# Performance work log

Measured on AMD Instinct MI355X. Metric: run time of the kernel, lower is better.

## Reference

```python
import jax, jax.numpy as jnp
import numpy as np

B = 32          # patients
D = 128         # hidden dim (modality_embedding_dim == total_hidden_dim)
H = 4           # attention heads
DH = D // H     # per-head dim
L = 2           # num_graph_layers
N = {'ct': 1024, 'pet': 1024, 'clin': 256, 'gen': 2048, 'pat': 1}
# (src_type, dst_type) for the 8 relation types registered in _setup_relations
REL = [('ct','ct'), ('pet','pet'), ('clin','clin'), ('gen','gen'),
       ('pat','clin'), ('ct','gen'), ('pet','gen'), ('gen','pat')]
E_REL = [8192, 8192, 2048, 16384, 256, 8192, 8192, 2048]
EDGE_NAMES = ['e_ct','e_pet','e_clin','e_gen','e_pat2clin','e_ct2gen','e_pet2gen','e_gen2pat']


def setup_inputs() -> dict:
    key = jax.random.key(0)
    ks = iter(jax.random.split(key, 64))
    nk = lambda: next(ks)
    inp = {}
    inp['x_ct']   = jax.random.normal(nk(), (B, N['ct'],  D), jnp.float32)
    inp['x_pet']  = jax.random.normal(nk(), (B, N['pet'], D), jnp.float32)
    inp['x_clin'] = jax.random.normal(nk(), (B, N['clin'],D), jnp.float32)
    inp['x_gen']  = jax.random.normal(nk(), (B, N['gen'], D), jnp.float32)
    inp['early']  = jax.random.normal(nk(), (B, D), jnp.float32)

    def mk_edges(k, E, ns, nd):
        k1, k2 = jax.random.split(k)
        src = jax.random.randint(k1, (B, 1, E), 0, ns, jnp.int32)
        dst = jax.random.randint(k2, (B, 1, E), 0, nd, jnp.int32)
        return jnp.concatenate([src, dst], axis=1)  # [B,2,E]

    for nm, (s, d), E in zip(EDGE_NAMES, REL, E_REL):
        inp[nm] = mk_edges(nk(), E, N[s], N[d])

    sw = 1.0 / np.sqrt(D)
    inp['W_src'] = jax.random.normal(nk(), (L, 8, D, D), jnp.float32) * sw
    inp['W_dst'] = jax.random.normal(nk(), (L, 8, D, D), jnp.float32) * sw
    inp['a_src'] = jax.random.normal(nk(), (L, 8, H, DH), jnp.float32) * sw
    inp['a_dst'] = jax.random.normal(nk(), (L, 8, H, DH), jnp.float32) * sw
    inp['Wp'] = jax.random.normal(nk(), (3, D, D), jnp.float32) * sw  # CT, PET, genomic pooling
    inp['bp'] = jnp.zeros((3, D), jnp.float32)
    inp['W_sem'] = jax.random.normal(nk(), (4 * D, 128), jnp.float32) * (1.0 / np.sqrt(4 * D))
    inp['b_sem'] = jnp.zeros((128,), jnp.float32)
    inp['q_sem'] = jax.random.normal(nk(), (128,), jnp.float32) * sw
    return inp


def _leaky_relu(x):
    return jnp.where(x > 0, x, 0.2 * x)


def _gat_layer(x, edges, Ws, Wd, As, Ad):
    """One heterogeneous multi-head GAT layer summing over relation types."""
    agg = {t: jnp.zeros((B, N[t], H, DH), jnp.float32) for t in N}
    for r, ((s, d), ei) in enumerate(zip(REL, edges)):
        hs = jnp.einsum('bnd,de->bne', x[s], Ws[r]).reshape(B, N[s], H, DH)
        hd = jnp.einsum('bnd,de->bne', x[d], Wd[r]).reshape(B, N[d], H, DH)
        al_s = jnp.sum(hs * As[r], axis=-1)  # [B,Ns,H]
        al_d = jnp.sum(hd * Ad[r], axis=-1)  # [B,Nd,H]
        nd = N[d]

        def one(hs_b, as_b, ad_b, e_b):
            src, dst = e_b[0], e_b[1]
            logit = _leaky_relu(as_b[src] + ad_b[dst])                      # [E,H]
            m = jnp.full((nd, H), -1e30, logit.dtype).at[dst].max(logit)    # segment max
            p = jnp.exp(logit - m[dst])
            den = jnp.zeros((nd, H), p.dtype).at[dst].add(p)
            w = p / (den[dst] + 1e-16)                                      # edge softmax per dst node
            msg = w[:, :, None] * hs_b[src]                                 # [E,H,DH]
            return jnp.zeros((nd, H, DH), msg.dtype).at[dst].add(msg)

        agg[d] = agg[d] + jax.vmap(one)(hs, al_s, al_d, ei)
    return {t: jax.nn.elu(agg[t].reshape(B, N[t], D)) for t in N}


def _pool(feat, W, b):
    # query = Linear(mean(features)); scores = feat @ q; softmax-weighted sum
    q = jnp.mean(feat, axis=1) @ W + b            # [B,D]
    sc = jnp.einsum('bnd,bd->bn', feat, q)        # [B,N]
    w = jax.nn.softmax(sc, axis=1)
    return jnp.einsum('bn,bnd->bd', w, feat)      # [B,D]


def _forward(x_ct, x_pet, x_clin, x_gen, early, edges,
             W_src, W_dst, a_src, a_dst, Wp, bp, W_sem, b_sem, q_sem):
    x = {'ct': x_ct, 'pet': x_pet, 'clin': x_clin, 'gen': x_gen,
         'pat': early[:, None, :]}
    for l in range(L):
        x = _gat_layer(x, edges, W_src[l], W_dst[l], a_src[l], a_dst[l])
    ct_p  = _pool(x['ct'],  Wp[0], bp[0])
    pet_p = _pool(x['pet'], Wp[1], bp[1])
    gen_p = _pool(x['gen'], Wp[2], bp[2])   # shared across the 3 meta-paths
    pad = jnp.zeros((B, 2 * D), ct_p.dtype)  # pad 2D -> 4D as in original
    imm = jnp.concatenate([ct_p, gen_p, pad], axis=1)
    pro = jnp.concatenate([pet_p, gen_p, pad], axis=1)
    trt = jnp.concatenate([(ct_p + pet_p) * 0.5, gen_p, pad], axis=1)
    z = jnp.stack([imm, pro, trt], axis=1)                     # [B,3,4D]
    s = jnp.einsum('bpa,a->bp', jnp.tanh(jnp.einsum('bpf,fa->bpa', z, W_sem) + b_sem), q_sem)
    beta = jax.nn.softmax(s, axis=1)                           # [B,3]
    fused = jnp.einsum('bp,bpf->bf', beta, z)                  # [B,4D]
    return fused, beta


def reference(x_ct, x_pet, x_clin, x_gen, early,
              e_ct, e_pet, e_clin, e_gen, e_pat2clin, e_ct2gen, e_pet2gen, e_gen2pat,
              W_src, W_dst, a_src, a_dst, Wp, bp, W_sem, b_sem, q_sem):
    edges = [e_ct, e_pet, e_clin, e_gen, e_pat2clin, e_ct2gen, e_pet2gen, e_gen2pat]
    return _forward(x_ct, x_pet, x_clin, x_gen, early, edges,
                    W_src, W_dst, a_src, a_dst, Wp, bp, W_sem, b_sem, q_sem)
```

## Files before the change

kernel.cpp:

```cpp
#include <hip/hip_runtime.h>
#include <math.h>

static constexpr int NB = 32;
static constexpr int ND = 128;

typedef short bf16x8 __attribute__((ext_vector_type(8)));
typedef float f32x4  __attribute__((ext_vector_type(4)));
typedef unsigned short u16x8 __attribute__((ext_vector_type(8)));

__device__ __forceinline__ float lrelu(float x){ return x > 0.f ? x : 0.2f*x; }
__device__ __forceinline__ unsigned short f2b(float f){
  unsigned u = __float_as_uint(f);
  return (unsigned short)((u + 0x7FFFu + ((u>>16)&1u)) >> 16);
}
__device__ __forceinline__ float b2f(unsigned short b){
  return __uint_as_float(((unsigned)b) << 16);
}

__global__ __launch_bounds__(128) void k_fold(const float* __restrict__ Wsrc,
    const float* __restrict__ Wdst, const float* __restrict__ asrc,
    const float* __restrict__ adst, float* __restrict__ vbuf){
  const int wid[5] = {0,1,3,5,6};
  int lr = blockIdx.x, role = blockIdx.y, l = blockIdx.z;
  int r = wid[lr];
  const float* W = (role ? Wdst : Wsrc) + (size_t)(l*8+r)*16384;
  const float* a = (role ? adst : asrc) + (size_t)(l*8+r)*128;
  int k = threadIdx.x;
  float* o = vbuf + ((size_t)((l*5+lr)*2+role))*512 + k*4;
  #pragma unroll
  for(int h=0;h<4;h++){
    float s = 0.f;
    #pragma unroll
    for(int j=0;j<32;j++) s += W[k*128 + h*32 + j]*a[h*32 + j];
    o[h] = s;
  }
}

__global__ __launch_bounds__(256) void k_wpack(const float* __restrict__ Wsrc,
    unsigned short* __restrict__ Wf){
  const int wid[5] = {0,1,3,5,6};
  int lr = blockIdx.x, l = blockIdx.y;
  const float* W = Wsrc + (size_t)(l*8+wid[lr])*16384;
  unsigned short* o = Wf + (size_t)((l*5+lr)*4)*4096;
  for(int idx=threadIdx.x; idx<128*128; idx+=256){
    int k = idx >> 7, col = idx & 127;
    int h = col >> 5, cc = col & 31;
    int k4 = k>>2, g = k4&3, kk = k4>>3, j = 4*((k4>>2)&1) + (k&3);
    int nb = cc>>4, lane = (cc&15) + 16*g;
    o[(size_t)h*4096 + ((size_t)((kk*2+nb)*64 + lane))*8 + j] = f2b(W[k*128 + col]);
  }
}

struct CsrP {
  const int* eg[5];
  int l2E[5];
  int Nd_[5];
  int roff_[5];
  int eoff_[5];
};

__global__ __launch_bounds__(512) void k_csr(CsrP P, int* __restrict__ rowstart,
                                             int* __restrict__ srcidx){
  int b = blockIdx.x, r = blockIdx.y, t = threadIdx.x;
  int E = 1<<P.l2E[r], Nd = P.Nd_[r];
  const int* eg = P.eg[r] + (size_t)b*2*E;
  int* rsO = rowstart + P.roff_[r] + b*(Nd+1);
  int* siO = srcidx + P.eoff_[r] + (size_t)b*E;
  __shared__ int cnt[2048];
  __shared__ int stmp[512];
  for(int i=t;i<Nd;i+=512) cnt[i]=0;
  __syncthreads();
  for(int e=t;e<E;e+=512) atomicAdd(&cnt[eg[E+e]], 1);
  __syncthreads();
  int carry=0;
  for(int c0=0;c0<Nd;c0+=512){
    int idx=c0+t;
    int v=(idx<Nd)?cnt[idx]:0;
    stmp[t]=v; __syncthreads();
    for(int off=1;off<512;off<<=1){
      int u=(t>=off)?stmp[t-off]:0;
      __syncthreads();
      stmp[t]+=u;
      __syncthreads();
    }
    int excl=stmp[t]-v+carry;
    if(idx<Nd){ rsO[idx]=excl; cnt[idx]=excl; }
    int tot = stmp[511];
    __syncthreads();
    carry+=tot;
  }
  if(t==0) rsO[Nd]=carry;
  __syncthreads();
  for(int e=t;e<E;e+=512){
    int src=eg[e], dst=eg[E+e];
    int pos=atomicAdd(&cnt[dst],1);
    siO[pos]=src;
  }
}

struct HsP {
  int tb[4];
  int usef;
  const float* xf[3];
  unsigned long long xoff[3];
  int Ns[3];
  int nW[3];
  unsigned long long wfo[3][2];
  unsigned long long hso[3][2];
  unsigned long long aso[3][2];
  unsigned long long asrco[3][2];
  int nvd[3];
  unsigned long long vdo[3][3];
  unsigned long long aldo2[3][3];
  int ndd[3][3];
};

__global__ __launch_bounds__(256) void k_hs(HsP P, const unsigned short* __restrict__ x16,
    const unsigned short* __restrict__ Wf, const float* __restrict__ asrc,
    const float* __restrict__ vbuf, unsigned short* __restrict__ hs,
    float* __restrict__ als, float* __restrict__ ald){
  __shared__ unsigned short xl[16*132];
  int B = blockIdx.x;
  int t=0; while(t<2 && B>=P.tb[t+1]) t++;
  int local = B - P.tb[t];
  int b = local & 31, tile = local >> 5;
  int n0 = tile*16;
  int tid = threadIdx.x, w = tid>>6, ln = tid&63;
  if(P.usef){
    const float* xf = P.xf[t] + ((size_t)((size_t)b*P.Ns[t] + n0))*128;
    int row = tid>>4, c8 = tid&15;
    float4 a = *(const float4*)(xf + (size_t)row*128 + c8*8);
    float4 c = *(const float4*)(xf + (size_t)row*128 + c8*8 + 4);
    u16x8 r;
    r[0]=f2b(a.x); r[1]=f2b(a.y); r[2]=f2b(a.z); r[3]=f2b(a.w);
    r[4]=f2b(c.x); r[5]=f2b(c.y); r[6]=f2b(c.z); r[7]=f2b(c.w);
    *(u16x8*)&xl[row*132 + c8*8] = r;
  } else {
    int row = tid>>4, ch = tid&15;
    u16x8 v = *(const u16x8*)(x16 + P.xoff[t] + ((size_t)((size_t)b*P.Ns[t] + n0+row)*128 + ch*8));
    *(u16x8*)&xl[row*132 + ch*8] = v;
  }
  __syncthreads();
  int g = ln>>4, r15 = ln&15;
  for(int rep=0; rep<P.nW[t]; rep++){
    const unsigned short* wf = Wf + P.wfo[t][rep] + (size_t)w*4096;
    f32x4 acc[2]; acc[0]=(f32x4){0,0,0,0}; acc[1]=(f32x4){0,0,0,0};
    #pragma unroll
    for(int kk=0;kk<4;kk++){
      const unsigned short* pa = &xl[r15*132 + kk*32 + 4*g];
      ushort4 lo = *(const ushort4*)pa;
      ushort4 hi = *(const ushort4*)(pa+16);
      union { ushort u[8]; bf16x8 v; } tmp;
      tmp.u[0]=lo.x; tmp.u[1]=lo.y; tmp.u[2]=lo.z; tmp.u[3]=lo.w;
      tmp.u[4]=hi.x; tmp.u[5]=hi.y; tmp.u[6]=hi.z; tmp.u[7]=hi.w;
      bf16x8 af = tmp.v;
      #pragma unroll
      for(int nb=0;nb<2;nb++){
        bf16x8 bw = *(const bf16x8*)(wf + ((size_t)((kk*2+nb)*64 + ln))*8);
        acc[nb] = __builtin_amdgcn_mfma_f32_16x16x32_bf16(af, bw, acc[nb], 0, 0, 0);
      }
    }
    unsigned short* ho = hs + P.hso[t][rep] + ((size_t)b*P.Ns[t] + n0)*128;
    #pragma unroll
    for(int qq=0;qq<4;qq++){
      int m = 4*g + qq;
      #pragma unroll
      for(int nb=0;nb<2;nb++){
        ho[(size_t)m*128 + w*32 + nb*16 + r15] = f2b(acc[nb][qq]);
      }
    }
    {
      const float* aS = asrc + P.asrco[t][rep];
      float a0v = aS[w*32 + r15], a1v = aS[w*32 + 16 + r15];
      float p0 = acc[0][0]*a0v + acc[1][0]*a1v;
      float p1 = acc[0][1]*a0v + acc[1][1]*a1v;
      float p2 = acc[0][2]*a0v + acc[1][2]*a1v;
      float p3 = acc[0][3]*a0v + acc[1][3]*a1v;
      #pragma unroll
      for(int off=1; off<16; off<<=1){
        p0 += __shfl_xor(p0,off); p1 += __shfl_xor(p1,off);
        p2 += __shfl_xor(p2,off); p3 += __shfl_xor(p3,off);
      }
      if(r15 < 4){
        float pv = (r15==0)?p0:((r15==1)?p1:((r15==2)?p2:p3));
        als[P.aso[t][rep] + ((size_t)b*P.Ns[t] + n0 + 4*g + r15)*4 + w] = pv;
      }
    }
  }
  int nvd = P.nvd[t];
  if(tid < (nvd<<6)){
    int vd = tid>>6, rem = tid&63, row = rem>>2, h = rem&3;
    const float* vv = vbuf + P.vdo[t][vd];
    float s = 0.f;
    #pragma unroll 8
    for(int k=0;k<128;k++) s += b2f(xl[row*132+k]) * vv[k*4+h];
    ald[P.aldo2[t][vd] + ((size_t)b*P.ndd[t][vd] + n0 + row)*4 + h] = s;
  }
}

static constexpr int MAXE4 = 1536;
static constexpr int WST4  = 1548;

struct Fu5P {
  int nrel[3], ndshift[3];
  int roff[3][3], eoff[3][3], E[3][3], Ns[3][3];
  int rowbase[3][3];
  unsigned long long aldo[3][3];
  unsigned long long outoff[3];
};

__global__ __launch_bounds__(512, 8) void k_fuse5(Fu5P P,
    const int* __restrict__ rowstart, const int* __restrict__ srcidx,
    const float* __restrict__ als, const float* __restrict__ ald,
    const unsigned short* __restrict__ hs, unsigned short* __restrict__ out16){
  __shared__ float wlds[4*WST4];
  __shared__ int   silds[MAXE4];
  __shared__ float aldl[3*256];
  __shared__ int   rsl[3*65];
  __shared__ int   crs[65];
  __shared__ int   cst[3*64];
  int B = blockIdx.x;
  int xcd = B & 7, slot = B >> 3;
  int bg = slot >> 6, rem = slot & 63;
  int b = bg*8 + xcd;
  int t, dtile;
  if(rem < 32){ t = 0; dtile = rem; }
  else if(rem < 48){ t = 1; dtile = rem - 32; }
  else { t = 2; dtile = rem - 48; }
  int Nd = 1 << P.ndshift[t];
  int d0 = dtile * 64;
  int tid = threadIdx.x, w = tid>>6, ln = tid&63;
  int nrel = P.nrel[t];

  for(int q=0;q<nrel;q++){
    const int* rsq = rowstart + P.roff[t][q] + b*(Nd+1) + d0;
    for(int i=tid;i<65;i+=512) rsl[q*65+i] = rsq[i];
    const float* aldq = ald + P.aldo[t][q] + ((size_t)b*Nd + d0)*4;
    for(int i=tid;i<256;i+=512) aldl[(q<<8)+i] = aldq[i];
  }
  __syncthreads();
  if(tid < 65){
    int s = 0;
    for(int q=0;q<nrel;q++) s += rsl[q*65+tid] - rsl[q*65];
    crs[tid] = s;
  } else if(tid >= 128 && tid < 128 + nrel*64){
    int q = (tid-128)>>6, d = (tid-128)&63;
    int s = 0;
    for(int q2=0;q2<nrel;q2++) s += rsl[q2*65+d] - rsl[q2*65];
    for(int q2=0;q2<q;q2++)    s += rsl[q2*65+d+1] - rsl[q2*65+d];
    cst[q*64+d] = s;
  }
  __syncthreads();
  for(int s=tid; s<(nrel<<8); s+=512){
    int q = s>>8, r2 = s&255, dloc = r2>>2, j = r2&3;
    const int* si = srcidx + P.eoff[t][q] + (size_t)b*P.E[t][q];
    int rs0 = rsl[q*65+dloc];
    int deg = rsl[q*65+dloc+1] - rs0;
    int cb = cst[q*64+dloc];
    int bake = P.rowbase[t][q] + b*P.Ns[t][q];
    for(int i=j;i<deg;i+=4) silds[cb+i] = bake + si[rs0+i];
  }
  __syncthreads();
  for(int s=tid; s<(nrel<<8); s+=512){
    int q = s>>8, r2 = s&255, dloc = r2>>2, j = r2&3;
    int deg = rsl[q*65+dloc+1] - rsl[q*65+dloc];
    int cb = cst[q*64+dloc];
    float4 ad4 = *(const float4*)&aldl[(q<<8)+(dloc<<2)];
    for(int i=j;i<deg;i+=4){
      int e = cb+i;
      int sil = silds[e];
      float4 as4 = *(const float4*)(als + 4*(size_t)sil);
      wlds[0*WST4+e] = lrelu(as4.x+ad4.x);
      wlds[1*WST4+e] = lrelu(as4.y+ad4.y);
      wlds[2*WST4+e] = lrelu(as4.z+ad4.z);
      wlds[3*WST4+e] = lrelu(as4.w+ad4.w);
    }
  }
  __syncthreads();
  for(int s=tid; s<(nrel<<8); s+=512){
    int q = s>>8, r2 = s&255, dloc = r2>>2, h2 = r2&3;
    int e0 = cst[q*64+dloc];
    int e1 = e0 + rsl[q*65+dloc+1] - rsl[q*65+dloc];
    float* wrow = &wlds[h2*WST4];
    float m = -1e30f;
    for(int e=e0;e<e1;e++) m = fmaxf(m, wrow[e]);
    float den = 0.f;
    for(int e=e0;e<e1;e++){ float p=__expf(wrow[e]-m); wrow[e]=p; den+=p; }
    float inv = 1.f/(den + 1e-16f);
    for(int e=e0;e<e1;e++) wrow[e] *= inv;
  }
  __syncthreads();
  int h = ln>>4;
  float accA[8], accB[8];
  #pragma unroll
  for(int i=0;i<8;i++){ accA[i]=0.f; accB[i]=0.f; }
  #pragma unroll
  for(int it=0; it<8; it++){
    int dloc = w*8 + it;
    int e0 = crs[dloc], e1 = crs[dloc+1];
    float a0 = 0.f, a1 = 0.f;
    int e = e0;
    int eal = (e0+3)&~3; if(eal > e1) eal = e1;
    for(; e<eal; e++){
      float wv = wlds[h*WST4 + e];
      unsigned v = *(const unsigned*)(hs + ((size_t)silds[e]*128 + 2*ln));
      a0 += wv*__uint_as_float(v<<16);
      a1 += wv*__uint_as_float(v&0xFFFF0000u);
    }
    for(; e+8<=e1; e+=8){
      int4  sq0 = *(const int4*)&silds[e];
      int4  sq1 = *(const int4*)&silds[e+4];
      float4 wq0 = *(const float4*)&wlds[h*WST4 + e];
      float4 wq1 = *(const float4*)&wlds[h*WST4 + e + 4];
      unsigned v0 = *(const unsigned*)(hs + ((size_t)sq0.x*128 + 2*ln));
      unsigned v1 = *(const unsigned*)(hs + ((size_t)sq0.y*128 + 2*ln));
      unsigned v2 = *(const unsigned*)(hs + ((size_t)sq0.z*128 + 2*ln));
      unsigned v3 = *(const unsigned*)(hs + ((size_t)sq0.w*128 + 2*ln));
      unsigned v4 = *(const unsigned*)(hs + ((size_t)sq1.x*128 + 2*ln));
      unsigned v5 = *(const unsigned*)(hs + ((size_t)sq1.y*128 + 2*ln));
      unsigned v6 = *(const unsigned*)(hs + ((size_t)sq1.z*128 + 2*ln));
      unsigned v7 = *(const unsigned*)(hs + ((size_t)sq1.w*128 + 2*ln));
      a0 += wq0.x*__uint_as_float(v0<<16); a1 += wq0.x*__uint_as_float(v0&0xFFFF0000u);
      a0 += wq0.y*__uint_as_float(v1<<16); a1 += wq0.y*__uint_as_float(v1&0xFFFF0000u);
      a0 += wq0.z*__uint_as_float(v2<<16); a1 += wq0.z*__uint_as_float(v2&0xFFFF0000u);
      a0 += wq0.w*__uint_as_float(v3<<16); a1 += wq0.w*__uint_as_float(v3&0xFFFF0000u);
      a0 += wq1.x*__uint_as_float(v4<<16); a1 += wq1.x*__uint_as_float(v4&0xFFFF0000u);
      a0 += wq1.y*__uint_as_float(v5<<16); a1 += wq1.y*__uint_as_float(v5&0xFFFF0000u);
      a0 += wq1.z*__uint_as_float(v6<<16); a1 += wq1.z*__uint_as_float(v6&0xFFFF0000u);
      a0 += wq1.w*__uint_as_float(v7<<16); a1 += wq1.w*__uint_as_float(v7&0xFFFF0000u);
    }
    for(; e+4<=e1; e+=4){
      int4  sq = *(const int4*)&silds[e];
      float4 wq = *(const float4*)&wlds[h*WST4 + e];
      unsigned v0 = *(const unsigned*)(hs + ((size_t)sq.x*128 + 2*ln));
      unsigned v1 = *(const unsigned*)(hs + ((size_t)sq.y*128 + 2*ln));
      unsigned v2 = *(const unsigned*)(hs + ((size_t)sq.z*128 + 2*ln));
      unsigned v3 = *(const unsigned*)(hs + ((size_t)sq.w*128 + 2*ln));
      a0 += wq.x*__uint_as_float(v0<<16); a1 += wq.x*__uint_as_float(v0&0xFFFF0000u);
      a0 += wq.y*__uint_as_float(v1<<16); a1 += wq.y*__uint_as_float(v1&0xFFFF0000u);
      a0 += wq.z*__uint_as_float(v2<<16); a1 += wq.z*__uint_as_float(v2&0xFFFF0000u);
      a0 += wq.w*__uint_as_float(v3<<16); a1 += wq.w*__uint_as_float(v3&0xFFFF0000u);
    }
    for(; e<e1; e++){
      float wv = wlds[h*WST4 + e];
      unsigned v = *(const unsigned*)(hs + ((size_t)silds[e]*128 + 2*ln));
      a0 += wv*__uint_as_float(v<<16);
      a1 += wv*__uint_as_float(v&0xFFFF0000u);
    }
    accA[it] = a0; accB[it] = a1;
  }
  #pragma unroll
  for(int it=0; it<8; it++){
    int m = d0 + w*8 + it;
    float v0 = accA[it], v1 = accB[it];
    v0 = v0 > 0.f ? v0 : expm1f(v0);
    v1 = v1 > 0.f ? v1 : expm1f(v1);
    ushort2 o; o.x = f2b(v0); o.y = f2b(v1);
    *(ushort2*)(out16 + P.outoff[t] + ((size_t)b*Nd + m)*128 + 2*ln) = o;
  }
}

__device__ __constant__ const size_t POFF[3] = {0ull, 4194304ull, 8388608ull};
__device__ __constant__ const int    PNN[3]  = {1024, 1024, 2048};
static constexpr int PCH = 64;
static constexpr int MAXCH = 32;

__global__ __launch_bounds__(128) void k_pool_psum(const unsigned short* __restrict__ x2,
    float* __restrict__ part){
  int p = blockIdx.z, b = blockIdx.x, c = blockIdx.y, t = threadIdx.x;
  int Nn = PNN[p];
  if(c*PCH >= Nn) return;
  const unsigned short* f = x2 + POFF[p] + ((size_t)b*Nn + c*PCH)*ND;
  float acc = 0.f;
  #pragma unroll 8
  for(int n=0;n<PCH;n++) acc += b2f(f[(size_t)n*ND + t]);
  part[(((size_t)p*NB + b)*MAXCH + c)*ND + t] = acc;
}

__global__ __launch_bounds__(128) void k_pool_q(const float* __restrict__ part,
    const float* __restrict__ Wp, const float* __restrict__ bp,
    float* __restrict__ q){
  int p = blockIdx.z, b = blockIdx.x, t = threadIdx.x;
  int nch = PNN[p]/PCH;
  __shared__ float mean[ND];
  float s = 0.f;
  for(int c=0;c<nch;c++) s += part[(((size_t)p*NB + b)*MAXCH + c)*ND + t];
  mean[t] = s / (float)PNN[p];
  __syncthreads();
  const float* W = Wp + (size_t)p*ND*ND;
  float qv = bp[p*ND + t];
  #pragma unroll 8
  for(int k=0;k<ND;k++) qv += mean[k]*W[k*ND + t];
  q[((size_t)p*NB + b)*ND + t] = qv;
}

__global__ __launch_bounds__(256) void k_pool_score(const unsigned short* __restrict__ x2,
    const float* __restrict__ q, float* __restrict__ sc){
  int p = blockIdx.z, b = blockIdx.y;
  int w = threadIdx.x >> 6, lane = threadIdx.x & 63;
  int n = blockIdx.x*4 + w;
  int Nn = PNN[p];
  if(n >= Nn) return;
  const unsigned short* f  = x2 + POFF[p] + ((size_t)b*Nn + n)*ND;
  const float* qb = q + ((size_t)p*NB + b)*ND;
  float s = b2f(f[lane])*qb[lane] + b2f(f[lane+64])*qb[lane+64];
  #pragma unroll
  for(int off=32; off; off>>=1) s += __shfl_xor(s, off);
  if(lane == 0) sc[((size_t)p*NB + b)*2048 + n] = s;
}

__global__ __launch_bounds__(256) void k_pool_smax(const float* __restrict__ sc,
    float* __restrict__ stat){
  int p = blockIdx.z, b = blockIdx.x, t = threadIdx.x;
  int Nn = PNN[p];
  __shared__ float red[256];
  const float* s = sc + ((size_t)p*NB + b)*2048;
  float mx = -1e30f;
  for(int n=t;n<Nn;n+=256) mx = fmaxf(mx, s[n]);
  red[t] = mx; __syncthreads();
  for(int o=128;o;o>>=1){ if(t<o) red[t]=fmaxf(red[t],red[t+o]); __syncthreads(); }
  mx = red[0]; __syncthreads();
  float sum = 0.f;
  for(int n=t;n<Nn;n+=256) sum += __expf(s[n]-mx);
  red[t] = sum; __syncthreads();
  for(int o=128;o;o>>=1){ if(t<o) red[t]+=red[t+o]; __syncthreads(); }
  if(t==0){ stat[((size_t)p*NB + b)*2] = mx; stat[((size_t)p*NB + b)*2+1] = 1.f/red[0]; }
}

__global__ __launch_bounds__(128) void k_pool_wsum(const unsigned short* __restrict__ x2,
    const float* __restrict__ sc, const float* __restrict__ stat,
    float* __restrict__ part){
  int p = blockIdx.z, b = blockIdx.x, c = blockIdx.y, t = threadIdx.x;
  int Nn = PNN[p];
  if(c*PCH >= Nn) return;
  __shared__ float wsh[PCH];
  float mx  = stat[((size_t)p*NB + b)*2];
  float inv = stat[((size_t)p*NB + b)*2+1];
  if(t < PCH) wsh[t] = __expf(sc[((size_t)p*NB + b)*2048 + c*PCH + t] - mx)*inv;
  __syncthreads();
  const unsigned short* f = x2 + POFF[p] + ((size_t)b*Nn + c*PCH)*ND;
  float acc = 0.f;
  #pragma unroll 8
  for(int n=0;n<PCH;n++) acc += wsh[n]*b2f(f[(size_t)n*ND + t]);
  part[(((size_t)p*NB + b)*MAXCH + c)*ND + t] = acc;
}

__global__ __launch_bounds__(128) void k_pool_comb(const float* __restrict__ part,
    float* __restrict__ pooled){
  int p = blockIdx.z, b = blockIdx.x, t = threadIdx.x;
  int nch = PNN[p]/PCH;
  float s = 0.f;
  for(int c=0;c<nch;c++) s += part[(((size_t)p*NB + b)*MAXCH + c)*ND + t];
  pooled[((size_t)p*NB + b)*ND + t] = s;
}

__global__ __launch_bounds__(128) void k_sem(const float* __restrict__ ctp,
    const float* __restrict__ petp, const float* __restrict__ genp,
    const float* __restrict__ Wsem, const float* __restrict__ bsem,
    const float* __restrict__ qsem, float* __restrict__ fused, float* __restrict__ beta){
  int b = blockIdx.x, t = threadIdx.x;
  __shared__ float z[3][256];
  __shared__ float red[128];
  float ct = ctp[b*ND + t], pet = petp[b*ND + t], gen = genp[b*ND + t];
  z[0][t]=ct;  z[1][t]=pet; z[2][t]=0.5f*(ct+pet);
  z[0][ND+t]=gen; z[1][ND+t]=gen; z[2][ND+t]=gen;
  __syncthreads();
  float s[3];
  for(int p=0;p<3;p++){
    float a = bsem[t];
    for(int f=0;f<256;f++) a += z[p][f]*Wsem[f*128 + t];
    a = tanhf(a);
    red[t] = a * qsem[t];
    __syncthreads();
    for(int o=64;o>0;o>>=1){ if(t<o) red[t]+=red[t+o]; __syncthreads(); }
    s[p] = red[0]; __syncthreads();
  }
  float mx = fmaxf(s[0], fmaxf(s[1], s[2]));
  float e0 = __expf(s[0]-mx), e1 = __expf(s[1]-mx), e2 = __expf(s[2]-mx);
  float sm = e0+e1+e2;
  float b0 = e0/sm, b1 = e1/sm, b2 = e2/sm;
  if(t < 3) beta[b*3 + t] = (t==0)?b0:((t==1)?b1:b2);
  float f0 = b0*z[0][t] + b1*z[1][t] + b2*z[2][t];
  float f1 = b0*z[0][ND+t] + b1*z[1][ND+t] + b2*z[2][ND+t];
  fused[(size_t)b*512 + t]       = f0;
  fused[(size_t)b*512 + 128 + t] = f1;
  fused[(size_t)b*512 + 256 + t] = 0.f;
  fused[(size_t)b*512 + 384 + t] = 0.f;
}

extern "C" void kernel_launch(void* const* d_in, const int* in_sizes, int n_in,
                              void* d_out, int out_size, void* d_ws, size_t ws_size,
                              hipStream_t stream) {
  static const int wid[5]    = {0,1,3,5,6};
  static const int edgein[5] = {5,6,8,10,11};
  static const int l2E[5]    = {13,13,14,13,13};
  static const int Nd_l[5]   = {1024,1024,2048,2048,2048};
  static const int E_l[5]    = {8192,8192,16384,8192,8192};
  static const int Ns_l[5]   = {1024,1024,2048,1024,1024};
  static const int eoff[6]   = {0,262144,524288,1048576,1310720,1572864};
  static const int roff[5]   = {0,32800,65600,131168,196736};
  static const unsigned long long aoff[5]   = {0,131072,262144,524288,655360};
  static const unsigned long long aldoff[5] = {0,131072,262144,524288,786432};
  static const unsigned long long hsoff_lr[5] = {0ull,4194304ull,8388608ull,16777216ull,20971520ull};
  static const unsigned long long ALD = 786432;

  const float* Wsrc = (const float*)d_in[13];
  const float* Wp   = (const float*)d_in[17];
  const float* bp   = (const float*)d_in[18];
  const float* Wsem = (const float*)d_in[19];
  const float* bsem = (const float*)d_in[20];
  const float* qsem = (const float*)d_in[21];

  unsigned short* xc16 = (unsigned short*)d_ws;
  unsigned short* x2b16 = xc16;
  unsigned short* xmid16 = xc16 + 16777216;
  float* albase = (float*)(xmid16 + 16777216);
  float* als = albase;
  float* ald = albase + ALD;
  float* vbuf = albase + 1835008;
  unsigned short* wfbuf = (unsigned short*)(vbuf + 10240);
  float* pooled = (float*)(wfbuf + 163840);
  float* part = pooled + 12288;
  float* qbuf = part + 393216;
  float* scbuf = qbuf + 12288;
  float* stat = scbuf + 196608;
  int* rowstart = (int*)(stat + 192);
  int* srcidx = rowstart + 262304;
  unsigned short* hs16 = (unsigned short*)(srcidx + 1572864);

  { dim3 g(5,2,2); k_fold<<<g,128,0,stream>>>(Wsrc, (const float*)d_in[14],
                                              (const float*)d_in[15], (const float*)d_in[16], vbuf); }
  { dim3 g(5,2); k_wpack<<<g,256,0,stream>>>(Wsrc, wfbuf); }

  CsrP csr;
  for(int r=0;r<5;r++){
    csr.eg[r] = (const int*)d_in[edgein[r]];
    csr.l2E[r] = l2E[r]; csr.Nd_[r] = Nd_l[r];
    csr.roff_[r] = roff[r]; csr.eoff_[r] = eoff[r];
  }
  { dim3 g(NB,5); k_csr<<<g,512,0,stream>>>(csr, rowstart, srcidx); }

  static const unsigned long long xoo[3] = {0,4194304,8388608};
  static const int t2_nrel[3] = {3,1,1};
  static const int t2_lrel[3][3] = {{2,3,4},{0,0,0},{1,0,0}};
  static const int t2_nds[3] = {11,10,10};
  static const int t2_out[3] = {2,0,1};

  Fu5P fp;
  for(int t=0;t<3;t++){
    fp.nrel[t]=t2_nrel[t]; fp.ndshift[t]=t2_nds[t]; fp.outoff[t]=xoo[t2_out[t]];
    for(int q=0;q<3;q++){
      int lr = t2_lrel[t][q];
      fp.roff[t][q]=roff[lr]; fp.eoff[t][q]=eoff[lr];
      fp.E[t][q]=E_l[lr]; fp.Ns[t][q]=Ns_l[lr];
      fp.rowbase[t][q]=(int)(aoff[lr]/4);
      fp.aldo[t][q]=aldoff[lr];
    }
  }

  static const int hs_lr[3][2] = {{0,3},{1,4},{2,2}};
  static const int vd_lr[3][3] = {{0,0,0},{1,0,0},{2,3,4}};
  HsP hp;
  hp.tb[0]=0; hp.tb[1]=2048; hp.tb[2]=4096; hp.tb[3]=8192;
  hp.xf[0]=(const float*)d_in[0]; hp.xf[1]=(const float*)d_in[1]; hp.xf[2]=(const float*)d_in[3];
  hp.xoff[0]=0; hp.xoff[1]=4194304; hp.xoff[2]=8388608;
  hp.Ns[0]=1024; hp.Ns[1]=1024; hp.Ns[2]=2048;
  hp.nW[0]=2; hp.nW[1]=2; hp.nW[2]=1;
  hp.nvd[0]=1; hp.nvd[1]=1; hp.nvd[2]=3;
  for(int t=0;t<3;t++){
    for(int rep=0;rep<2;rep++){
      int lr = hs_lr[t][rep];
      hp.hso[t][rep]=hsoff_lr[lr];
      hp.aso[t][rep]=aoff[lr];
    }
    for(int vd=0;vd<3;vd++){
      int lr = vd_lr[t][vd];
      hp.aldo2[t][vd]=aldoff[lr];
      hp.ndd[t][vd]=Nd_l[lr];
    }
  }
  hp.hso[2][1]=0; hp.aso[2][1]=0;

  for(int l=0;l<2;l++){
    unsigned short* xout = (l==0) ? xmid16 : x2b16;
    hp.usef = (l==0) ? 1 : 0;

    for(int t=0;t<3;t++){
      for(int rep=0;rep<2;rep++){
        int lr = hs_lr[t][rep];
        hp.wfo[t][rep]=(unsigned long long)((l*5 + lr)*4)*4096;
        hp.asrco[t][rep]=(unsigned long long)((l*8 + wid[lr])*128);
      }
      for(int vd=0;vd<3;vd++){
        int lr = vd_lr[t][vd];
        hp.vdo[t][vd]=((unsigned long long)((l*5+lr)*2+1))*512;
      }
    }
    k_hs<<<8192,256,0,stream>>>(hp, xmid16, wfbuf, (const float*)d_in[15], vbuf,
                                hs16, als, ald);

    k_fuse5<<<2048,512,0,stream>>>(fp, rowstart, srcidx, als, ald, hs16, xout);
  }

  {
    dim3 gchunk(NB, MAXCH, 3);
    dim3 gone(NB, 1, 3);
    dim3 gscore(512, NB, 3);
    k_pool_psum <<<gchunk,128,0,stream>>>(x2b16, part);
    k_pool_q    <<<gone,  128,0,stream>>>(part, Wp, bp, qbuf);
    k_pool_score<<<gscore,256,0,stream>>>(x2b16, qbuf, scbuf);
    k_pool_smax <<<gone,  256,0,stream>>>(scbuf, stat);
    k_pool_wsum <<<gchunk,128,0,stream>>>(x2b16, scbuf, stat, part);
    k_pool_comb <<<gone,  128,0,stream>>>(part, pooled);
  }

  float* fused = (float*)d_out;
  float* beta  = fused + (size_t)NB*512;
  k_sem<<<NB,128,0,stream>>>(pooled, pooled + NB*ND, pooled + 2*NB*ND,
                             Wsem, bsem, qsem, fused, beta);
}
```

Baseline: 336.0 us.

## Fuse pooling into one kernel, merge GAT softmax phases, wave-scan CSR

Three independent changes. The six attention-pooling kernels become a single per-(patient, modality) block of 1024 threads that computes the mean, the query, the scores, the softmax and the weighted sum without global round trips. The k_fuse5 edge-prep phases (index staging, logits, max, exp, normalize) collapse into one pass with per-row shuffle reductions, and the crs/cst tables are dropped in favour of recomputing offsets. The CSR prefix scan changes from a barrier-heavy shared-memory scan to per-thread chunks plus a wavefront shuffle scan. The risk is that the pooling grid of only 96 blocks underuses the GPU when streaming the large activation tensor.

```diff
diff --git a/kernel.cpp b/kernel.cpp
--- a/kernel.cpp
+++ b/kernel.cpp
@@ -67,29 +67,33 @@
   int* rsO = rowstart + P.roff_[r] + b*(Nd+1);
   int* siO = srcidx + P.eoff_[r] + (size_t)b*E;
   __shared__ int cnt[2048];
-  __shared__ int stmp[512];
+  __shared__ int wsums[8];
   for(int i=t;i<Nd;i+=512) cnt[i]=0;
   __syncthreads();
   for(int e=t;e<E;e+=512) atomicAdd(&cnt[eg[E+e]], 1);
   __syncthreads();
-  int carry=0;
-  for(int c0=0;c0<Nd;c0+=512){
-    int idx=c0+t;
-    int v=(idx<Nd)?cnt[idx]:0;
-    stmp[t]=v; __syncthreads();
-    for(int off=1;off<512;off<<=1){
-      int u=(t>=off)?stmp[t-off]:0;
-      __syncthreads();
-      stmp[t]+=u;
-      __syncthreads();
-    }
-    int excl=stmp[t]-v+carry;
-    if(idx<Nd){ rsO[idx]=excl; cnt[idx]=excl; }
-    int tot = stmp[511];
-    __syncthreads();
-    carry+=tot;
-  }
-  if(t==0) rsO[Nd]=carry;
+  int C = Nd >> 9;
+  int base = t*C;
+  int loc[4]; int s_=0;
+  for(int i=0;i<C;i++){ loc[i]=cnt[base+i]; s_+=loc[i]; }
+  int lane = t&63, wv = t>>6;
+  int sinc = s_;
+  #pragma unroll
+  for(int off=1;off<64;off<<=1){
+    int u = __shfl_up(sinc, off);
+    if(lane>=off) sinc += u;
+  }
+  if(lane==63) wsums[wv]=sinc;
+  __syncthreads();
+  int wbase=0, total=0;
+  #pragma unroll
+  for(int i=0;i<8;i++){ int v=wsums[i]; if(i<wv) wbase+=v; total+=v; }
+  int excl = wbase + sinc - s_;
+  for(int i=0;i<C;i++){
+    int idx=base+i;
+    rsO[idx]=excl; cnt[idx]=excl; excl+=loc[i];
+  }
+  if(t==0) rsO[Nd]=total;
   __syncthreads();
   for(int e=t;e<E;e+=512){
     int src=eg[e], dst=eg[E+e];
@@ -209,16 +213,13 @@
   unsigned long long outoff[3];
 };
 
-__global__ __launch_bounds__(512, 8) void k_fuse5(Fu5P P,
+__global__ __launch_bounds__(512, 8) void k_fuse6(Fu5P P,
     const int* __restrict__ rowstart, const int* __restrict__ srcidx,
     const float* __restrict__ als, const float* __restrict__ ald,
     const unsigned short* __restrict__ hs, unsigned short* __restrict__ out16){
   __shared__ float wlds[4*WST4];
   __shared__ int   silds[MAXE4];
-  __shared__ float aldl[3*256];
   __shared__ int   rsl[3*65];
-  __shared__ int   crs[65];
-  __shared__ int   cst[3*64];
   int B = blockIdx.x;
   int xcd = B & 7, slot = B >> 3;
   int bg = slot >> 6, rem = slot & 63;
@@ -235,61 +236,57 @@
   for(int q=0;q<nrel;q++){
     const int* rsq = rowstart + P.roff[t][q] + b*(Nd+1) + d0;
     for(int i=tid;i<65;i+=512) rsl[q*65+i] = rsq[i];
-    const float* aldq = ald + P.aldo[t][q] + ((size_t)b*Nd + d0)*4;
-    for(int i=tid;i<256;i+=512) aldl[(q<<8)+i] = aldq[i];
-  }
-  __syncthreads();
-  if(tid < 65){
-    int s = 0;
-    for(int q=0;q<nrel;q++) s += rsl[q*65+tid] - rsl[q*65];
-    crs[tid] = s;
-  } else if(tid >= 128 && tid < 128 + nrel*64){
-    int q = (tid-128)>>6, d = (tid-128)&63;
-    int s = 0;
-    for(int q2=0;q2<nrel;q2++) s += rsl[q2*65+d] - rsl[q2*65];
-    for(int q2=0;q2<q;q2++)    s += rsl[q2*65+d+1] - rsl[q2*65+d];
-    cst[q*64+d] = s;
-  }
-  __syncthreads();
+  }
+  __syncthreads();
+
   for(int s=tid; s<(nrel<<8); s+=512){
     int q = s>>8, r2 = s&255, dloc = r2>>2, j = r2&3;
-    const int* si = srcidx + P.eoff[t][q] + (size_t)b*P.E[t][q];
     int rs0 = rsl[q*65+dloc];
     int deg = rsl[q*65+dloc+1] - rs0;
-    int cb = cst[q*64+dloc];
+    int cb = 0;
+    for(int q2=0;q2<nrel;q2++) cb += rsl[q2*65+dloc] - rsl[q2*65];
+    for(int q2=0;q2<q;q2++)    cb += rsl[q2*65+dloc+1] - rsl[q2*65+dloc];
+    const int* si = srcidx + P.eoff[t][q] + (size_t)b*P.E[t][q];
     int bake = P.rowbase[t][q] + b*P.Ns[t][q];
-    for(int i=j;i<deg;i+=4) silds[cb+i] = bake + si[rs0+i];
-  }
-  __syncthreads();
-  for(int s=tid; s<(nrel<<8); s+=512){
-    int q = s>>8, r2 = s&255, dloc = r2>>2, j = r2&3;
-    int deg = rsl[q*65+dloc+1] - rsl[q*65+dloc];
-    int cb = cst[q*64+dloc];
-    float4 ad4 = *(const float4*)&aldl[(q<<8)+(dloc<<2)];
+    float4 ad4 = *(const float4*)(ald + P.aldo[t][q] + ((size_t)b*Nd + d0 + dloc)*4);
+    float m0=-1e30f,m1=-1e30f,m2=-1e30f,m3=-1e30f;
     for(int i=j;i<deg;i+=4){
       int e = cb+i;
-      int sil = silds[e];
+      int sil = bake + si[rs0+i];
+      silds[e] = sil;
       float4 as4 = *(const float4*)(als + 4*(size_t)sil);
-      wlds[0*WST4+e] = lrelu(as4.x+ad4.x);
-      wlds[1*WST4+e] = lrelu(as4.y+ad4.y);
-      wlds[2*WST4+e] = lrelu(as4.z+ad4.z);
-      wlds[3*WST4+e] = lrelu(as4.w+ad4.w);
-    }
-  }
-  __syncthreads();
-  for(int s=tid; s<(nrel<<8); s+=512){
-    int q = s>>8, r2 = s&255, dloc = r2>>2, h2 = r2&3;
-    int e0 = cst[q*64+dloc];
-    int e1 = e0 + rsl[q*65+dloc+1] - rsl[q*65+dloc];
-    float* wrow = &wlds[h2*WST4];
-    float m = -1e30f;
-    for(int e=e0;e<e1;e++) m = fmaxf(m, wrow[e]);
-    float den = 0.f;
-    for(int e=e0;e<e1;e++){ float p=__expf(wrow[e]-m); wrow[e]=p; den+=p; }
-    float inv = 1.f/(den + 1e-16f);
-    for(int e=e0;e<e1;e++) wrow[e] *= inv;
-  }
-  __syncthreads();
+      float l0=lrelu(as4.x+ad4.x), l1=lrelu(as4.y+ad4.y);
+      float l2=lrelu(as4.z+ad4.z), l3=lrelu(as4.w+ad4.w);
+      wlds[0*WST4+e]=l0; wlds[1*WST4+e]=l1;
+      wlds[2*WST4+e]=l2; wlds[3*WST4+e]=l3;
+      m0=fmaxf(m0,l0); m1=fmaxf(m1,l1); m2=fmaxf(m2,l2); m3=fmaxf(m3,l3);
+    }
+    m0=fmaxf(m0,__shfl_xor(m0,1)); m1=fmaxf(m1,__shfl_xor(m1,1));
+    m2=fmaxf(m2,__shfl_xor(m2,1)); m3=fmaxf(m3,__shfl_xor(m3,1));
+    m0=fmaxf(m0,__shfl_xor(m0,2)); m1=fmaxf(m1,__shfl_xor(m1,2));
+    m2=fmaxf(m2,__shfl_xor(m2,2)); m3=fmaxf(m3,__shfl_xor(m3,2));
+    float n0_=0.f,n1_=0.f,n2_=0.f,n3_=0.f;
+    for(int i=j;i<deg;i+=4){
+      int e = cb+i;
+      float p0=__expf(wlds[0*WST4+e]-m0); wlds[0*WST4+e]=p0; n0_+=p0;
+      float p1=__expf(wlds[1*WST4+e]-m1); wlds[1*WST4+e]=p1; n1_+=p1;
+      float p2=__expf(wlds[2*WST4+e]-m2); wlds[2*WST4+e]=p2; n2_+=p2;
+      float p3=__expf(wlds[3*WST4+e]-m3); wlds[3*WST4+e]=p3; n3_+=p3;
+    }
+    n0_+=__shfl_xor(n0_,1); n1_+=__shfl_xor(n1_,1);
+    n2_+=__shfl_xor(n2_,1); n3_+=__shfl_xor(n3_,1);
+    n0_+=__shfl_xor(n0_,2); n1_+=__shfl_xor(n1_,2);
+    n2_+=__shfl_xor(n2_,2); n3_+=__shfl_xor(n3_,2);
+    float i0=1.f/(n0_+1e-16f), i1=1.f/(n1_+1e-16f);
+    float i2=1.f/(n2_+1e-16f), i3=1.f/(n3_+1e-16f);
+    for(int i=j;i<deg;i+=4){
+      int e = cb+i;
+      wlds[0*WST4+e]*=i0; wlds[1*WST4+e]*=i1;
+      wlds[2*WST4+e]*=i2; wlds[3*WST4+e]*=i3;
+    }
+  }
+  __syncthreads();
+
   int h = ln>>4;
   float accA[8], accB[8];
   #pragma unroll
@@ -297,7 +294,12 @@
   #pragma unroll
   for(int it=0; it<8; it++){
     int dloc = w*8 + it;
-    int e0 = crs[dloc], e1 = crs[dloc+1];
+    int e0=0, e1=0;
+    for(int q2=0;q2<nrel;q2++){
+      int r0 = rsl[q2*65];
+      e0 += rsl[q2*65+dloc]   - r0;
+      e1 += rsl[q2*65+dloc+1] - r0;
+    }
     float a0 = 0.f, a1 = 0.f;
     int e = e0;
     int eal = (e0+3)&~3; if(eal > e1) eal = e1;
@@ -362,96 +364,82 @@
 
 __device__ __constant__ const size_t POFF[3] = {0ull, 4194304ull, 8388608ull};
 __device__ __constant__ const int    PNN[3]  = {1024, 1024, 2048};
-static constexpr int PCH = 64;
-static constexpr int MAXCH = 32;
-
-__global__ __launch_bounds__(128) void k_pool_psum(const unsigned short* __restrict__ x2,
-    float* __restrict__ part){
-  int p = blockIdx.z, b = blockIdx.x, c = blockIdx.y, t = threadIdx.x;
-  int Nn = PNN[p];
-  if(c*PCH >= Nn) return;
-  const unsigned short* f = x2 + POFF[p] + ((size_t)b*Nn + c*PCH)*ND;
-  float acc = 0.f;
-  #pragma unroll 8
-  for(int n=0;n<PCH;n++) acc += b2f(f[(size_t)n*ND + t]);
-  part[(((size_t)p*NB + b)*MAXCH + c)*ND + t] = acc;
-}
-
-__global__ __launch_bounds__(128) void k_pool_q(const float* __restrict__ part,
+
+__global__ __launch_bounds__(1024) void k_pool2(const unsigned short* __restrict__ x2,
     const float* __restrict__ Wp, const float* __restrict__ bp,
-    float* __restrict__ q){
-  int p = blockIdx.z, b = blockIdx.x, t = threadIdx.x;
-  int nch = PNN[p]/PCH;
-  __shared__ float mean[ND];
-  float s = 0.f;
-  for(int c=0;c<nch;c++) s += part[(((size_t)p*NB + b)*MAXCH + c)*ND + t];
-  mean[t] = s / (float)PNN[p];
-  __syncthreads();
-  const float* W = Wp + (size_t)p*ND*ND;
-  float qv = bp[p*ND + t];
-  #pragma unroll 8
-  for(int k=0;k<ND;k++) qv += mean[k]*W[k*ND + t];
-  q[((size_t)p*NB + b)*ND + t] = qv;
-}
-
-__global__ __launch_bounds__(256) void k_pool_score(const unsigned short* __restrict__ x2,
-    const float* __restrict__ q, float* __restrict__ sc){
-  int p = blockIdx.z, b = blockIdx.y;
-  int w = threadIdx.x >> 6, lane = threadIdx.x & 63;
-  int n = blockIdx.x*4 + w;
-  int Nn = PNN[p];
-  if(n >= Nn) return;
-  const unsigned short* f  = x2 + POFF[p] + ((size_t)b*Nn + n)*ND;
-  const float* qb = q + ((size_t)p*NB + b)*ND;
-  float s = b2f(f[lane])*qb[lane] + b2f(f[lane+64])*qb[lane+64];
-  #pragma unroll
-  for(int off=32; off; off>>=1) s += __shfl_xor(s, off);
-  if(lane == 0) sc[((size_t)p*NB + b)*2048 + n] = s;
-}
-
-__global__ __launch_bounds__(256) void k_pool_smax(const float* __restrict__ sc,
-    float* __restrict__ stat){
-  int p = blockIdx.z, b = blockIdx.x, t = threadIdx.x;
-  int Nn = PNN[p];
-  __shared__ float red[256];
-  const float* s = sc + ((size_t)p*NB + b)*2048;
-  float mx = -1e30f;
-  for(int n=t;n<Nn;n+=256) mx = fmaxf(mx, s[n]);
-  red[t] = mx; __syncthreads();
-  for(int o=128;o;o>>=1){ if(t<o) red[t]=fmaxf(red[t],red[t+o]); __syncthreads(); }
-  mx = red[0]; __syncthreads();
-  float sum = 0.f;
-  for(int n=t;n<Nn;n+=256) sum += __expf(s[n]-mx);
-  red[t] = sum; __syncthreads();
-  for(int o=128;o;o>>=1){ if(t<o) red[t]+=red[t+o]; __syncthreads(); }
-  if(t==0){ stat[((size_t)p*NB + b)*2] = mx; stat[((size_t)p*NB + b)*2+1] = 1.f/red[0]; }
-}
-
-__global__ __launch_bounds__(128) void k_pool_wsum(const unsigned short* __restrict__ x2,
-    const float* __restrict__ sc, const float* __restrict__ stat,
-    float* __restrict__ part){
-  int p = blockIdx.z, b = blockIdx.x, c = blockIdx.y, t = threadIdx.x;
-  int Nn = PNN[p];
-  if(c*PCH >= Nn) return;
-  __shared__ float wsh[PCH];
-  float mx  = stat[((size_t)p*NB + b)*2];
-  float inv = stat[((size_t)p*NB + b)*2+1];
-  if(t < PCH) wsh[t] = __expf(sc[((size_t)p*NB + b)*2048 + c*PCH + t] - mx)*inv;
-  __syncthreads();
-  const unsigned short* f = x2 + POFF[p] + ((size_t)b*Nn + c*PCH)*ND;
-  float acc = 0.f;
-  #pragma unroll 8
-  for(int n=0;n<PCH;n++) acc += wsh[n]*b2f(f[(size_t)n*ND + t]);
-  part[(((size_t)p*NB + b)*MAXCH + c)*ND + t] = acc;
-}
-
-__global__ __launch_bounds__(128) void k_pool_comb(const float* __restrict__ part,
     float* __restrict__ pooled){
-  int p = blockIdx.z, b = blockIdx.x, t = threadIdx.x;
-  int nch = PNN[p]/PCH;
-  float s = 0.f;
-  for(int c=0;c<nch;c++) s += part[(((size_t)p*NB + b)*MAXCH + c)*ND + t];
-  pooled[((size_t)p*NB + b)*ND + t] = s;
+  int b = blockIdx.x, p = blockIdx.y;
+  int tid = threadIdx.x;
+  int N = PNN[p];
+  const unsigned short* f = x2 + POFF[p] + (size_t)b*N*ND;
+  __shared__ float sc[2048];
+  __shared__ float psum[8*ND];
+  __shared__ float meanq[2*ND];
+  __shared__ float red[16];
+  int g = tid>>7, d = tid&127;
+  {
+    float acc=0.f;
+    for(int n=g;n<N;n+=8) acc += b2f(f[(size_t)n*ND+d]);
+    psum[g*ND+d]=acc;
+  }
+  __syncthreads();
+  if(tid<ND){
+    float s=0.f;
+    #pragma unroll
+    for(int gg=0;gg<8;gg++) s+=psum[gg*ND+tid];
+    meanq[tid]=s/(float)N;
+  }
+  __syncthreads();
+  if(tid<ND){
+    const float* W = Wp + (size_t)p*ND*ND;
+    float qv = bp[p*ND+tid];
+    #pragma unroll 8
+    for(int k=0;k<ND;k++) qv += meanq[k]*W[k*ND+tid];
+    meanq[ND+tid]=qv;
+  }
+  __syncthreads();
+  float mx_l = -1e30f;
+  for(int n=tid;n<N;n+=1024){
+    const unsigned short* fr = f + (size_t)n*ND;
+    float s=0.f;
+    for(int k=0;k<ND;k+=8){
+      u16x8 v = *(const u16x8*)(fr+k);
+      #pragma unroll
+      for(int jj=0;jj<8;jj++) s += b2f((unsigned short)v[jj])*meanq[ND+k+jj];
+    }
+    sc[n]=s; mx_l=fmaxf(mx_l,s);
+  }
+  #pragma unroll
+  for(int off=32;off;off>>=1) mx_l=fmaxf(mx_l,__shfl_xor(mx_l,off));
+  if((tid&63)==0) red[tid>>6]=mx_l;
+  __syncthreads();
+  float mx=red[0];
+  #pragma unroll
+  for(int i=1;i<16;i++) mx=fmaxf(mx,red[i]);
+  __syncthreads();
+  float den_l=0.f;
+  for(int n=tid;n<N;n+=1024){ float e=__expf(sc[n]-mx); sc[n]=e; den_l+=e; }
+  #pragma unroll
+  for(int off=32;off;off>>=1) den_l += __shfl_xor(den_l,off);
+  if((tid&63)==0) red[tid>>6]=den_l;
+  __syncthreads();
+  float den=0.f;
+  #pragma unroll
+  for(int i=0;i<16;i++) den+=red[i];
+  float inv=1.f/den;
+  __syncthreads();
+  {
+    float acc=0.f;
+    for(int n=g;n<N;n+=8) acc += sc[n]*b2f(f[(size_t)n*ND+d]);
+    psum[g*ND+d]=acc;
+  }
+  __syncthreads();
+  if(tid<ND){
+    float s=0.f;
+    #pragma unroll
+    for(int gg=0;gg<8;gg++) s+=psum[gg*ND+tid];
+    pooled[((size_t)p*NB+b)*ND+tid]=s*inv;
+  }
 }
 
 __global__ __launch_bounds__(128) void k_sem(const float* __restrict__ ctp,
@@ -521,10 +509,7 @@
   unsigned short* wfbuf = (unsigned short*)(vbuf + 10240);
   float* pooled = (float*)(wfbuf + 163840);
   float* part = pooled + 12288;
-  float* qbuf = part + 393216;
-  float* scbuf = qbuf + 12288;
-  float* stat = scbuf + 196608;
-  int* rowstart = (int*)(stat + 192);
+  int* rowstart = (int*)(part + 393216 + 12288 + 196608 + 192);
   int* srcidx = rowstart + 262304;
   unsigned short* hs16 = (unsigned short*)(srcidx + 1572864);
 
@@ -599,20 +584,10 @@
     k_hs<<<8192,256,0,stream>>>(hp, xmid16, wfbuf, (const float*)d_in[15], vbuf,
                                 hs16, als, ald);
 
-    k_fuse5<<<2048,512,0,stream>>>(fp, rowstart, srcidx, als, ald, hs16, xout);
-  }
-
-  {
-    dim3 gchunk(NB, MAXCH, 3);
-    dim3 gone(NB, 1, 3);
-    dim3 gscore(512, NB, 3);
-    k_pool_psum <<<gchunk,128,0,stream>>>(x2b16, part);
-    k_pool_q    <<<gone,  128,0,stream>>>(part, Wp, bp, qbuf);
-    k_pool_score<<<gscore,256,0,stream>>>(x2b16, qbuf, scbuf);
-    k_pool_smax <<<gone,  256,0,stream>>>(scbuf, stat);
-    k_pool_wsum <<<gchunk,128,0,stream>>>(x2b16, scbuf, stat, part);
-    k_pool_comb <<<gone,  128,0,stream>>>(part, pooled);
-  }
+    k_fuse6<<<2048,512,0,stream>>>(fp, rowstart, srcidx, als, ald, hs16, xout);
+  }
+
+  { dim3 g(NB,3); k_pool2<<<g,1024,0,stream>>>(x2b16, Wp, bp, pooled); }
 
   float* fused = (float*)d_out;
   float* beta  = fused + (size_t)NB*512;
```

Result: slower. 412.4 us (+22.7%).
